# Optimization experiments

Hardware: AMD Instinct MI355X
Metric: run time of the kernel (lower is better)

Reference implementation:

```python
import jax, jax.numpy as jnp
import numpy as np

HIDDEN = 512
HEADS = 8
HEAD_DIM = HIDDEN // HEADS   # 64
MAN_DIM = 256                # manifold_dim = hidden_dim // 2
SCALE = HEAD_DIM ** -0.5


def _c(re, im):
    return jax.lax.complex(re, im)


def setup_inputs() -> dict:
    key = jax.random.key(0)
    ks = jax.random.split(key, 13)
    def w(k, shape, fan_in):
        return (jax.random.normal(k, shape, dtype=jnp.float32) / np.sqrt(fan_in)).astype(jnp.float32)
    B, S = 2, 2048
    return {
        "x": jax.random.normal(ks[0], (B, S, HIDDEN), dtype=jnp.float32),
        "Wq_re": w(ks[1], (HIDDEN, HIDDEN), HIDDEN), "Wq_im": w(ks[2], (HIDDEN, HIDDEN), HIDDEN),
        "Wk_re": w(ks[3], (HIDDEN, HIDDEN), HIDDEN), "Wk_im": w(ks[4], (HIDDEN, HIDDEN), HIDDEN),
        "Wv_re": w(ks[5], (HIDDEN, HIDDEN), HIDDEN), "Wv_im": w(ks[6], (HIDDEN, HIDDEN), HIDDEN),
        "Wm_re": w(ks[7], (HEAD_DIM, MAN_DIM), HEAD_DIM), "Wm_im": w(ks[8], (HEAD_DIM, MAN_DIM), HEAD_DIM),
        "Wmi_re": w(ks[9], (MAN_DIM, HEAD_DIM), MAN_DIM), "Wmi_im": w(ks[10], (MAN_DIM, HEAD_DIM), MAN_DIM),
        "Wo_re": w(ks[11], (HIDDEN, HIDDEN), HIDDEN), "Wo_im": w(ks[12], (HIDDEN, HIDDEN), HIDDEN),
    }


def reference(x, Wq_re, Wq_im, Wk_re, Wk_im, Wv_re, Wv_im,
              Wm_re, Wm_im, Wmi_re, Wmi_im, Wo_re, Wo_im):
    B, S, D = x.shape
    # quantum state preparation: cast to complex, L2-normalize along last dim
    xc = x.astype(jnp.complex64)
    norm = jnp.linalg.norm(xc, axis=-1, keepdims=True)
    xc = xc / norm

    Wq, Wk, Wv = _c(Wq_re, Wq_im), _c(Wk_re, Wk_im), _c(Wv_re, Wv_im)
    Wm, Wmi, Wo = _c(Wm_re, Wm_im), _c(Wmi_re, Wmi_im), _c(Wo_re, Wo_im)

    def heads(t):  # [B,S,D] -> [B,H,S,head_dim]
        return t.reshape(B, S, HEADS, HEAD_DIM).transpose(0, 2, 1, 3)

    q = heads(xc @ Wq)
    k = heads(xc @ Wk)
    v = heads(xc @ Wv)

    # project each head onto the manifold (complex linear)
    qm = jnp.einsum('bhsd,dm->bhsm', q, Wm)
    km = jnp.einsum('bhsd,dm->bhsm', k, Wm)
    vm = jnp.einsum('bhsd,dm->bhsm', v, Wm)

    # Hermitian inner product attention scores; softmax over real part
    scores = jnp.einsum('bhqm,bhkm->bhqk', qm, jnp.conj(km)) * SCALE
    attn = jax.nn.softmax(scores.real, axis=-1).astype(jnp.complex64)

    outm = jnp.einsum('bhqk,bhkm->bhqm', attn, vm)
    out = jnp.einsum('bhsm,md->bhsd', outm, Wmi)        # back to head_dim
    out = out.transpose(0, 2, 1, 3).reshape(B, S, D)    # merge heads
    out = out @ Wo
    # return real/imag stacked as float32 (complex64 output -> [B,S,D,2])
    return jnp.stack([out.real, out.imag], axis=-1)
```

## Files before the change

### kernel.cpp

```cpp
#include <hip/hip_runtime.h>
#include <hip/hip_bf16.h>
#include <stdint.h>


typedef __attribute__((ext_vector_type(8))) short bf16x8;
typedef __attribute__((ext_vector_type(4))) float f32x4;

#define QSCALE 0.18033688011112042f

__device__ __forceinline__ unsigned short f2b(float f) {
    union { float f; unsigned int u; } v; v.f = f;
    unsigned int r = v.u + 0x7fffu + ((v.u >> 16) & 1u);
    return (unsigned short)(r >> 16);
}

__device__ __forceinline__ unsigned int cvtpk(float a, float b) {
    union { __hip_bfloat162 h; unsigned int u; } v;
    v.h = __float22bfloat162_rn(make_float2(a, b));
    return v.u;
}

__device__ __forceinline__ void ld16(void* lds, const void* g) {
    __builtin_amdgcn_global_load_lds(
        (__attribute__((address_space(1))) unsigned int*)(g),
        (__attribute__((address_space(3))) unsigned int*)(lds), 16, 0, 0);
}

__global__ __launch_bounds__(256) void k_prep(
        const float* __restrict__ x, unsigned short* __restrict__ xn,
        const float* __restrict__ s0, const float* __restrict__ s1,
        const float* __restrict__ s2, const float* __restrict__ s3,
        const float* __restrict__ s4, const float* __restrict__ s5,
        const float* __restrict__ s6, const float* __restrict__ s7,
        float* __restrict__ d0, float* __restrict__ d1,
        float* __restrict__ d2, float* __restrict__ d3,
        float* __restrict__ d4, float* __restrict__ d5,
        float* __restrict__ d6, float* __restrict__ d7) {
    __shared__ float tile[64][65];
    if (blockIdx.x < 1024) {
        int row  = blockIdx.x * 4 + (threadIdx.x >> 6);
        int lane = threadIdx.x & 63;
        const float4* xr = (const float4*)(x + (size_t)row * 512);
        float4 a = xr[lane], b = xr[lane + 64];
        float s = a.x*a.x + a.y*a.y + a.z*a.z + a.w*a.w
                + b.x*b.x + b.y*b.y + b.z*b.z + b.w*b.w;
        #pragma unroll
        for (int m = 1; m < 64; m <<= 1) s += __shfl_xor(s, m, 64);
        float inv = 1.0f / sqrtf(s);
        ushort4 o;
        o.x = f2b(a.x*inv); o.y = f2b(a.y*inv); o.z = f2b(a.z*inv); o.w = f2b(a.w*inv);
        *(ushort4*)&xn[(size_t)row*512 + lane*4] = o;
        o.x = f2b(b.x*inv); o.y = f2b(b.y*inv); o.z = f2b(b.z*inv); o.w = f2b(b.w*inv);
        *(ushort4*)&xn[(size_t)row*512 + 256 + lane*4] = o;
        return;
    }
    int bid = blockIdx.x - 1024;
    const float* src; float* dst; int R, C, tr, tc;
    if (bid < 384) {
        int mat = bid >> 6, tl = bid & 63;
        src = (mat==0)?s0:(mat==1)?s1:(mat==2)?s2:(mat==3)?s3:(mat==4)?s4:s5;
        dst = (mat==0)?d0:(mat==1)?d1:(mat==2)?d2:(mat==3)?d3:(mat==4)?d4:d5;
        R = 512; C = 512; tr = tl >> 3; tc = tl & 7;
    } else {
        int mat = (bid - 384) >> 2, tl = (bid - 384) & 3;
        src = mat ? s7 : s6; dst = mat ? d7 : d6;
        R = 64; C = 256; tr = 0; tc = tl;
    }
    int r0 = tr * 64, c0 = tc * 64;
    int tx = threadIdx.x & 63, ty = threadIdx.x >> 6;
    #pragma unroll
    for (int i = 0; i < 16; i++) {
        int r = ty + i*4;
        tile[r][tx] = src[(size_t)(r0 + r)*C + c0 + tx];
    }
    __syncthreads();
    #pragma unroll
    for (int i = 0; i < 16; i++) {
        int r = ty + i*4;
        dst[(size_t)(c0 + r)*R + r0 + tx] = tile[tx][r];
    }
}

__global__ __launch_bounds__(256) void k_gh(const float* __restrict__ Wm_re, const float* __restrict__ Wm_im,
                                            const float* __restrict__ WmT_re, const float* __restrict__ WmT_im,
                                            const float* __restrict__ Wmi_re, const float* __restrict__ Wmi_im,
                                            float* __restrict__ GH) {
    int id = blockIdx.x * 256 + threadIdx.x;
    int mat = id >> 12;
    int a = (id >> 6) & 63, c = id & 63;
    float s = 0.f;
    if (mat < 2) {
        for (int m = 0; m < 256; m++) {
            float ar = Wm_re[a*256+m], ai = Wm_im[a*256+m];
            float br = WmT_re[m*64+c], bi = WmT_im[m*64+c];
            s += (mat == 0) ? (ar*br + ai*bi) : (ai*br - ar*bi);
        }
        GH[id] = s;
    } else {
        for (int m = 0; m < 256; m++) {
            float ar = Wm_re[a*256+m], ai = Wm_im[a*256+m];
            float br = Wmi_re[m*64+c], bi = Wmi_im[m*64+c];
            s += (mat == 2) ? (ar*br - ai*bi) : (ar*bi + ai*br);
        }
        GH[mat*4096 + c*64 + a] = s;
    }
}

__global__ __launch_bounds__(256) void k_pack(
        const float* __restrict__ WqT_re, const float* __restrict__ WqT_im,
        const float* __restrict__ WkT_re, const float* __restrict__ WkT_im,
        const float* __restrict__ WvT_re, const float* __restrict__ WvT_im,
        const float* __restrict__ Wo_re,  const float* __restrict__ Wo_im,
        const float* __restrict__ GH,
        unsigned short* __restrict__ WqkvT, unsigned short* __restrict__ Wbig) {
    if (blockIdx.x < 6144) {
        int id = blockIdx.x * 256 + threadIdx.x;
        int n = id >> 9, k = id & 511;
        float val;
        if (n < 1024) {
            int h = n >> 7, part = (n >> 6) & 1, j = n & 63;
            const float* Gr = GH;
            const float* Gi = GH + 4096;
            const float* qr = WqT_re + (size_t)(h*64)*512 + k;
            const float* qi = WqT_im + (size_t)(h*64)*512 + k;
            float s = 0.f;
            if (part == 0) { for (int d = 0; d < 64; d++) s += qr[d*512]*Gr[d*64+j] - qi[d*512]*Gi[d*64+j]; }
            else           { for (int d = 0; d < 64; d++) s += qr[d*512]*Gi[d*64+j] + qi[d*512]*Gr[d*64+j]; }
            val = s * QSCALE;
        } else if (n < 2048) {
            int m = n - 1024; int h = m >> 7, part = (m >> 6) & 1, j = m & 63;
            val = (part ? WkT_im : WkT_re)[(size_t)(h*64+j)*512 + k];
        } else {
            int m = n - 2048; int h = m >> 7, part = (m >> 6) & 1, j = m & 63;
            val = (part ? WvT_im : WvT_re)[(size_t)(h*64+j)*512 + k];
        }
        WqkvT[id] = f2b(val);
    } else {
        int id = (blockIdx.x - 6144) * 256 + threadIdx.x;
        int np = id >> 10, kk = id & 1023;
        int c = np >> 1, p = np & 1;
        int h = kk >> 7, pp = (kk >> 6) & 1, d = kk & 63;
        const float* HrT = GH + 2*4096;
        const float* HiT = GH + 3*4096;
        float s = 0.f;
        if (p == pp) {
            for (int j = 0; j < 64; j++) {
                float hr = HrT[j*64+d], hi = HiT[j*64+d];
                float wr = Wo_re[(size_t)(h*64+j)*512 + c];
                float wi = Wo_im[(size_t)(h*64+j)*512 + c];
                s += hr*wr - hi*wi;
            }
        } else {
            for (int j = 0; j < 64; j++) {
                float hr = HrT[j*64+d], hi = HiT[j*64+d];
                float wr = Wo_re[(size_t)(h*64+j)*512 + c];
                float wi = Wo_im[(size_t)(h*64+j)*512 + c];
                s += hr*wi + hi*wr;
            }
            if (p == 0) s = -s;
        }
        Wbig[(size_t)np*1024 + kk] = f2b(s);
    }
}

template<int MODE, int MT>
__global__ __launch_bounds__(256, 2) void k_gemm(
        const unsigned short* __restrict__ Ain, const unsigned short* __restrict__ Btin,
        void* __restrict__ Cout, unsigned short* __restrict__ Vt, int K) {
    __shared__ __align__(16) unsigned short Al[MT*32];
    __shared__ __align__(16) unsigned short Bl[128*32];
    const int t = threadIdx.x;
    const int wave = t >> 6, lane = t & 63, quad = lane >> 4, l16 = lane & 15;
    const int wr = wave >> 1, wc = wave & 1;

    const unsigned short* A;
    const unsigned short* Bt;
    unsigned short* Cb = nullptr;
    int m0, n0;
    if (MODE == 0) {
        if (blockIdx.y < 16) {
            A = Ain; Bt = Btin;
            m0 = blockIdx.x * 128; n0 = blockIdx.y * 128;
            Cb = (unsigned short*)Cout;
        } else {
            int idx = (blockIdx.y - 16) * 32 + blockIdx.x;
            int b = idx >> 7, mt = (idx >> 4) & 7, nt = idx & 15;
            A  = Btin + 2048*512;
            Bt = Ain + (size_t)b*2048*512;
            m0 = mt * 128; n0 = nt * 128;
            Cb = Vt + (size_t)b*1024*2048;
        }
    } else {
        A = Ain; Bt = Btin;
        m0 = blockIdx.x * MT; n0 = blockIdx.y * 128;
    }

    f32x4 acc[MT/32][4] = {};
    for (int kt = 0; kt < K; kt += 32) {
        #pragma unroll
        for (int i = 0; i < MT/64; i++) {
            int g = t + i*256, r = g >> 2, gr = g & 3;
            ld16(&Al[g*8], &A[(size_t)(m0 + r)*K + kt + gr*8]);
        }
        #pragma unroll
        for (int i = 0; i < 2; i++) {
            int g = t + i*256, r = g >> 2, gr = g & 3;
            ld16(&Bl[g*8], &Bt[(size_t)(n0 + r)*K + kt + gr*8]);
        }
        __syncthreads();
        bf16x8 af[MT/32], bfr[4];
        #pragma unroll
        for (int rt = 0; rt < MT/32; rt++)
            af[rt] = *(const bf16x8*)&Al[(wr*(MT/2) + rt*16 + l16)*32 + quad*8];
        #pragma unroll
        for (int ct = 0; ct < 4; ct++)
            bfr[ct] = *(const bf16x8*)&Bl[(wc*64 + ct*16 + l16)*32 + quad*8];
        #pragma unroll
        for (int rt = 0; rt < MT/32; rt++)
            #pragma unroll
            for (int ct = 0; ct < 4; ct++)
                acc[rt][ct] = __builtin_amdgcn_mfma_f32_16x16x32_bf16(af[rt], bfr[ct], acc[rt][ct], 0, 0, 0);
        __syncthreads();
    }
    #pragma unroll
    for (int rt = 0; rt < MT/32; rt++) {
        int row = m0 + wr*(MT/2) + rt*16 + quad*4;
        #pragma unroll
        for (int ct = 0; ct < 4; ct++) {
            int col = n0 + wc*64 + ct*16 + l16;
            if (MODE == 0) {
                unsigned int u01 = cvtpk(acc[rt][ct][0], acc[rt][ct][1]);
                unsigned int u23 = cvtpk(acc[rt][ct][2], acc[rt][ct][3]);
                Cb[(size_t)(row+0)*2048 + col] = (unsigned short)(u01);
                Cb[(size_t)(row+1)*2048 + col] = (unsigned short)(u01 >> 16);
                Cb[(size_t)(row+2)*2048 + col] = (unsigned short)(u23);
                Cb[(size_t)(row+3)*2048 + col] = (unsigned short)(u23 >> 16);
            } else {
                float* C = (float*)Cout;
                #pragma unroll
                for (int r = 0; r < 4; r++)
                    C[(size_t)(row + r)*1024 + col] = acc[rt][ct][r];
            }
        }
    }
}

__global__ __launch_bounds__(256, 2) void k_attn(
        const unsigned short* __restrict__ QK,
        const unsigned short* __restrict__ Vt,
        unsigned short* __restrict__ O) {
    __shared__ __align__(16) unsigned short Kl[2][8192];
    __shared__ __align__(16) unsigned short Vl[2][8192];
    __shared__ __align__(16) unsigned short Pl[9216];

    const int t = threadIdx.x, wave = t >> 6, lane = t & 63, quad = lane >> 4, l16 = lane & 15;
    const int bh = blockIdx.x, b = bh >> 3, h = bh & 7;
    const int tok0 = b*2048 + blockIdx.y*128;

    bf16x8 qf[2][4];
    #pragma unroll
    for (int rt = 0; rt < 2; rt++)
        #pragma unroll
        for (int ks = 0; ks < 4; ks++)
            qf[rt][ks] = *(const bf16x8*)&QK[(size_t)(tok0 + wave*32 + rt*16 + l16)*2048 + h*128 + ks*32 + quad*8];

    const int key = t >> 2, gr = t & 3;
    const unsigned short* kp  = QK + (size_t)(b*2048 + key)*2048 + 1024 + h*128 + gr*8;
    const unsigned short* vp0 = Vt + (size_t)(b*1024 + h*128 + key)*2048 + gr*8;
    const unsigned short* vp1 = Vt + (size_t)(b*1024 + h*128 + 64 + key)*2048 + gr*8;

    f32x4 Oacc[2][8] = {};
    float ls[2][4] = {};

    {
        size_t ko = 0;
        #pragma unroll
        for (int i = 0; i < 4; i++) ld16(&Kl[0][(i*256 + t)*8], kp + ko + i*32);
        #pragma unroll
        for (int i = 0; i < 4; i++) ld16(&Vl[0][(i*256 + t)*8], ((i & 1) ? vp1 : vp0) + (i >> 1)*32);
    }
    __syncthreads();

    for (int it = 0; it < 32; it++) {
        const int cur = it & 1;
        if (it < 31) {
            int kt = (it + 1) * 64;
            size_t ko = (size_t)kt * 2048;
            #pragma unroll
            for (int i = 0; i < 4; i++) ld16(&Kl[cur^1][(i*256 + t)*8], kp + ko + i*32);
            #pragma unroll
            for (int i = 0; i < 4; i++) ld16(&Vl[cur^1][(i*256 + t)*8], ((i & 1) ? vp1 : vp0) + kt + (i >> 1)*32);
        }

        f32x4 S[2][4] = {};
        #pragma unroll
        for (int ks = 0; ks < 4; ks++) {
            #pragma unroll
            for (int ct = 0; ct < 4; ct++) {
                bf16x8 kf = *(const bf16x8*)&Kl[cur][ks*2048 + (ct*16 + l16)*32 + quad*8];
                #pragma unroll
                for (int rt = 0; rt < 2; rt++)
                    S[rt][ct] = __builtin_amdgcn_mfma_f32_16x16x32_bf16(qf[rt][ks], kf, S[rt][ct], 0, 0, 0);
            }
        }
        #pragma unroll
        for (int rt = 0; rt < 2; rt++) {
            #pragma unroll
            for (int ct = 0; ct < 4; ct++) {
                float p0 = exp2f(S[rt][ct][0]), p1 = exp2f(S[rt][ct][1]);
                float p2 = exp2f(S[rt][ct][2]), p3 = exp2f(S[rt][ct][3]);
                ls[rt][0] += p0; ls[rt][1] += p1; ls[rt][2] += p2; ls[rt][3] += p3;
                int q = wave*32 + rt*16 + quad*4;
                int base = (ct >> 1)*4608 + (ct & 1)*16 + l16;
                unsigned int u01 = cvtpk(p0, p1);
                unsigned int u23 = cvtpk(p2, p3);
                Pl[base + (q+0)*36] = (unsigned short)(u01);
                Pl[base + (q+1)*36] = (unsigned short)(u01 >> 16);
                Pl[base + (q+2)*36] = (unsigned short)(u23);
                Pl[base + (q+3)*36] = (unsigned short)(u23 >> 16);
            }
        }
        #pragma unroll
        for (int ks2 = 0; ks2 < 2; ks2++) {
            bf16x8 pf[2];
            #pragma unroll
            for (int rt = 0; rt < 2; rt++)
                pf[rt] = *(const bf16x8*)&Pl[ks2*4608 + (wave*32 + rt*16 + l16)*36 + quad*8];
            #pragma unroll
            for (int dt = 0; dt < 8; dt++) {
                bf16x8 vf = *(const bf16x8*)&Vl[cur][ks2*4096 + (dt*16 + l16)*32 + quad*8];
                #pragma unroll
                for (int rt = 0; rt < 2; rt++)
                    Oacc[rt][dt] = __builtin_amdgcn_mfma_f32_16x16x32_bf16(pf[rt], vf, Oacc[rt][dt], 0, 0, 0);
            }
        }
        __syncthreads();
    }

    #pragma unroll
    for (int rt = 0; rt < 2; rt++)
        #pragma unroll
        for (int r = 0; r < 4; r++) {
            float s = ls[rt][r];
            #pragma unroll
            for (int m = 1; m < 16; m <<= 1) s += __shfl_xor(s, m, 64);
            ls[rt][r] = 1.0f / s;
        }
    #pragma unroll
    for (int rt = 0; rt < 2; rt++) {
        int tok = tok0 + wave*32 + rt*16 + quad*4;
        #pragma unroll
        for (int dt = 0; dt < 8; dt++) {
            int col = h*128 + dt*16 + l16;
            unsigned int u01 = cvtpk(Oacc[rt][dt][0]*ls[rt][0], Oacc[rt][dt][1]*ls[rt][1]);
            unsigned int u23 = cvtpk(Oacc[rt][dt][2]*ls[rt][2], Oacc[rt][dt][3]*ls[rt][3]);
            O[(size_t)(tok+0)*1024 + col] = (unsigned short)(u01);
            O[(size_t)(tok+1)*1024 + col] = (unsigned short)(u01 >> 16);
            O[(size_t)(tok+2)*1024 + col] = (unsigned short)(u23);
            O[(size_t)(tok+3)*1024 + col] = (unsigned short)(u23 >> 16);
        }
    }
}

extern "C" void kernel_launch(void* const* d_in, const int* in_sizes, int n_in,
                              void* d_out, int out_size, void* d_ws, size_t ws_size,
                              hipStream_t stream) {
    (void)in_sizes; (void)n_in; (void)out_size; (void)ws_size;
    const float* x      = (const float*)d_in[0];
    const float* Wq_re  = (const float*)d_in[1];
    const float* Wq_im  = (const float*)d_in[2];
    const float* Wk_re  = (const float*)d_in[3];
    const float* Wk_im  = (const float*)d_in[4];
    const float* Wv_re  = (const float*)d_in[5];
    const float* Wv_im  = (const float*)d_in[6];
    const float* Wm_re  = (const float*)d_in[7];
    const float* Wm_im  = (const float*)d_in[8];
    const float* Wmi_re = (const float*)d_in[9];
    const float* Wmi_im = (const float*)d_in[10];
    const float* Wo_re  = (const float*)d_in[11];
    const float* Wo_im  = (const float*)d_in[12];

    char* ws = (char*)d_ws;
    unsigned short* xn    = (unsigned short*)(ws);
    unsigned short* WqkvT = (unsigned short*)(ws + (4u << 20));
    unsigned short* Wbig  = (unsigned short*)(ws + (7u << 20));
    float*          GH    = (float*)         (ws + (9u << 20));
    float*          WmT_re= (float*)         (ws + (9u << 20) + (64u << 10));
    float*          WmT_im= (float*)         (ws + (9u << 20) + (128u << 10));
    unsigned short* QK    = (unsigned short*)(ws + (10u << 20));
    unsigned short* Vt    = (unsigned short*)(ws + (26u << 20));
    unsigned short* Obuf  = (unsigned short*)(ws + (34u << 20));
    float* WqT_re = (float*)(ws + (10u << 20));
    float* WqT_im = (float*)(ws + (11u << 20));
    float* WkT_re = (float*)(ws + (12u << 20));
    float* WkT_im = (float*)(ws + (13u << 20));
    float* WvT_re = (float*)(ws + (14u << 20));
    float* WvT_im = (float*)(ws + (15u << 20));

    k_prep      <<<dim3(1416), dim3(256), 0, stream>>>(
        x, xn,
        Wq_re, Wq_im, Wk_re, Wk_im, Wv_re, Wv_im, Wm_re, Wm_im,
        WqT_re, WqT_im, WkT_re, WkT_im, WvT_re, WvT_im, WmT_re, WmT_im);
    k_gh        <<<dim3(64),   dim3(256), 0, stream>>>(Wm_re, Wm_im, WmT_re, WmT_im, Wmi_re, Wmi_im, GH);
    k_pack      <<<dim3(10240),dim3(256), 0, stream>>>(
        WqT_re, WqT_im, WkT_re, WkT_im, WvT_re, WvT_im, Wo_re, Wo_im, GH, WqkvT, Wbig);
    k_gemm<0,128><<<dim3(32, 24), dim3(256), 0, stream>>>(xn, WqkvT, (void*)QK, Vt, 512);
    k_attn      <<<dim3(16, 16), dim3(256), 0, stream>>>(QK, Vt, Obuf);
    k_gemm<1,64> <<<dim3(64, 8), dim3(256), 0, stream>>>(Obuf, Wbig, d_out, nullptr, 1024);
}
```

Measured before the change: 271.6 us.

## Split attention keys across two wave groups per block and merge partial results

The attention kernel now runs 512 threads per block, split into two groups of four waves that each handle half of the 2048 keys for the same 128 queries. The partial output accumulators and row sums are merged through shared memory at the end. V fragments are now read directly from global memory into registers instead of being staged through LDS. The goal is more waves in flight per block to hide latency on a 256-block grid. The cost is a final merge pass, higher register pressure and uncoalesced V loads from global memory.

```diff
diff --git a/kernel.cpp b/kernel.cpp
--- a/kernel.cpp
+++ b/kernel.cpp
@@ -245,15 +245,17 @@
     }
 }
 
-__global__ __launch_bounds__(256, 2) void k_attn(
+__global__ __launch_bounds__(512, 2) void k_attn(
         const unsigned short* __restrict__ QK,
         const unsigned short* __restrict__ Vt,
         unsigned short* __restrict__ O) {
-    __shared__ __align__(16) unsigned short Kl[2][8192];
-    __shared__ __align__(16) unsigned short Vl[2][8192];
-    __shared__ __align__(16) unsigned short Pl[9216];
-
-    const int t = threadIdx.x, wave = t >> 6, lane = t & 63, quad = lane >> 4, l16 = lane & 15;
+    __shared__ __align__(16) unsigned short Kl[2][2][8192];
+    __shared__ __align__(16) unsigned short Pl[2][9216];
+
+    const int t = threadIdx.x;
+    const int wave = t >> 6, g = wave >> 2, w = wave & 3;
+    const int lane = t & 63, quad = lane >> 4, l16 = lane & 15;
+    const int gt = t & 255;
     const int bh = blockIdx.x, b = bh >> 3, h = bh & 7;
     const int tok0 = b*2048 + blockIdx.y*128;
 
@@ -262,42 +264,41 @@
     for (int rt = 0; rt < 2; rt++)
         #pragma unroll
         for (int ks = 0; ks < 4; ks++)
-            qf[rt][ks] = *(const bf16x8*)&QK[(size_t)(tok0 + wave*32 + rt*16 + l16)*2048 + h*128 + ks*32 + quad*8];
-
-    const int key = t >> 2, gr = t & 3;
-    const unsigned short* kp  = QK + (size_t)(b*2048 + key)*2048 + 1024 + h*128 + gr*8;
-    const unsigned short* vp0 = Vt + (size_t)(b*1024 + h*128 + key)*2048 + gr*8;
-    const unsigned short* vp1 = Vt + (size_t)(b*1024 + h*128 + 64 + key)*2048 + gr*8;
+            qf[rt][ks] = *(const bf16x8*)&QK[(size_t)(tok0 + w*32 + rt*16 + l16)*2048 + h*128 + ks*32 + quad*8];
+
+    const int skey = gt >> 2, sgr = gt & 3;
+    const unsigned short* kp = QK + (size_t)(b*2048 + g*1024 + skey)*2048 + 1024 + h*128 + sgr*8;
+    const unsigned short* vbase = Vt + (size_t)(b*1024 + h*128)*2048 + g*1024;
 
     f32x4 Oacc[2][8] = {};
     float ls[2][4] = {};
 
-    {
-        size_t ko = 0;
-        #pragma unroll
-        for (int i = 0; i < 4; i++) ld16(&Kl[0][(i*256 + t)*8], kp + ko + i*32);
-        #pragma unroll
-        for (int i = 0; i < 4; i++) ld16(&Vl[0][(i*256 + t)*8], ((i & 1) ? vp1 : vp0) + (i >> 1)*32);
-    }
+    #pragma unroll
+    for (int i = 0; i < 4; i++)
+        ld16(&Kl[g][0][(i*256 + gt)*8], kp + i*32);
     __syncthreads();
 
-    for (int it = 0; it < 32; it++) {
+    for (int it = 0; it < 16; it++) {
         const int cur = it & 1;
-        if (it < 31) {
-            int kt = (it + 1) * 64;
-            size_t ko = (size_t)kt * 2048;
-            #pragma unroll
-            for (int i = 0; i < 4; i++) ld16(&Kl[cur^1][(i*256 + t)*8], kp + ko + i*32);
-            #pragma unroll
-            for (int i = 0; i < 4; i++) ld16(&Vl[cur^1][(i*256 + t)*8], ((i & 1) ? vp1 : vp0) + kt + (i >> 1)*32);
-        }
+        const int kt = it * 64;
+        if (it < 15) {
+            #pragma unroll
+            for (int i = 0; i < 4; i++)
+                ld16(&Kl[g][cur^1][(i*256 + gt)*8], kp + (size_t)(kt + 64)*2048 + i*32);
+        }
+        bf16x8 vf[2][8];
+        #pragma unroll
+        for (int ks2 = 0; ks2 < 2; ks2++)
+            #pragma unroll
+            for (int dt = 0; dt < 8; dt++)
+                vf[ks2][dt] = *(const bf16x8*)&vbase[(size_t)(dt*16 + l16)*2048 + kt + ks2*32 + quad*8];
 
         f32x4 S[2][4] = {};
         #pragma unroll
         for (int ks = 0; ks < 4; ks++) {
             #pragma unroll
             for (int ct = 0; ct < 4; ct++) {
-                bf16x8 kf = *(const bf16x8*)&Kl[cur][ks*2048 + (ct*16 + l16)*32 + quad*8];
+                bf16x8 kf = *(const bf16x8*)&Kl[g][cur][ks*2048 + (ct*16 + l16)*32 + quad*8];
                 #pragma unroll
                 for (int rt = 0; rt < 2; rt++)
                     S[rt][ct] = __builtin_amdgcn_mfma_f32_16x16x32_bf16(qf[rt][ks], kf, S[rt][ct], 0, 0, 0);
@@ -310,14 +311,14 @@
                 float p0 = exp2f(S[rt][ct][0]), p1 = exp2f(S[rt][ct][1]);
                 float p2 = exp2f(S[rt][ct][2]), p3 = exp2f(S[rt][ct][3]);
                 ls[rt][0] += p0; ls[rt][1] += p1; ls[rt][2] += p2; ls[rt][3] += p3;
-                int q = wave*32 + rt*16 + quad*4;
+                int q = w*32 + rt*16 + quad*4;
                 int base = (ct >> 1)*4608 + (ct & 1)*16 + l16;
                 unsigned int u01 = cvtpk(p0, p1);
                 unsigned int u23 = cvtpk(p2, p3);
-                Pl[base + (q+0)*36] = (unsigned short)(u01);
-                Pl[base + (q+1)*36] = (unsigned short)(u01 >> 16);
-                Pl[base + (q+2)*36] = (unsigned short)(u23);
-                Pl[base + (q+3)*36] = (unsigned short)(u23 >> 16);
+                Pl[g][base + (q+0)*36] = (unsigned short)(u01);
+                Pl[g][base + (q+1)*36] = (unsigned short)(u01 >> 16);
+                Pl[g][base + (q+2)*36] = (unsigned short)(u23);
+                Pl[g][base + (q+3)*36] = (unsigned short)(u23 >> 16);
             }
         }
         #pragma unroll
@@ -325,14 +326,12 @@
             bf16x8 pf[2];
             #pragma unroll
             for (int rt = 0; rt < 2; rt++)
-                pf[rt] = *(const bf16x8*)&Pl[ks2*4608 + (wave*32 + rt*16 + l16)*36 + quad*8];
-            #pragma unroll
-            for (int dt = 0; dt < 8; dt++) {
-                bf16x8 vf = *(const bf16x8*)&Vl[cur][ks2*4096 + (dt*16 + l16)*32 + quad*8];
+                pf[rt] = *(const bf16x8*)&Pl[g][ks2*4608 + (w*32 + rt*16 + l16)*36 + quad*8];
+            #pragma unroll
+            for (int dt = 0; dt < 8; dt++)
                 #pragma unroll
                 for (int rt = 0; rt < 2; rt++)
-                    Oacc[rt][dt] = __builtin_amdgcn_mfma_f32_16x16x32_bf16(pf[rt], vf, Oacc[rt][dt], 0, 0, 0);
-            }
+                    Oacc[rt][dt] = __builtin_amdgcn_mfma_f32_16x16x32_bf16(pf[rt], vf[ks2][dt], Oacc[rt][dt], 0, 0, 0);
         }
         __syncthreads();
     }
@@ -344,20 +343,47 @@
             float s = ls[rt][r];
             #pragma unroll
             for (int m = 1; m < 16; m <<= 1) s += __shfl_xor(s, m, 64);
-            ls[rt][r] = 1.0f / s;
-        }
-    #pragma unroll
-    for (int rt = 0; rt < 2; rt++) {
-        int tok = tok0 + wave*32 + rt*16 + quad*4;
-        #pragma unroll
-        for (int dt = 0; dt < 8; dt++) {
-            int col = h*128 + dt*16 + l16;
-            unsigned int u01 = cvtpk(Oacc[rt][dt][0]*ls[rt][0], Oacc[rt][dt][1]*ls[rt][1]);
-            unsigned int u23 = cvtpk(Oacc[rt][dt][2]*ls[rt][2], Oacc[rt][dt][3]*ls[rt][3]);
-            O[(size_t)(tok+0)*1024 + col] = (unsigned short)(u01);
-            O[(size_t)(tok+1)*1024 + col] = (unsigned short)(u01 >> 16);
-            O[(size_t)(tok+2)*1024 + col] = (unsigned short)(u23);
-            O[(size_t)(tok+3)*1024 + col] = (unsigned short)(u23 >> 16);
+            ls[rt][r] = s;
+        }
+
+    float* mergeO = (float*)&Kl[0][0][0];
+    float* mergeL = (float*)&Pl[1][0];
+    if (g == 1) {
+        #pragma unroll
+        for (int rt = 0; rt < 2; rt++) {
+            int q = w*32 + rt*16 + quad*4;
+            #pragma unroll
+            for (int r = 0; r < 4; r++) mergeL[q + r] = ls[rt][r];
+            #pragma unroll
+            for (int dt = 0; dt < 8; dt++)
+                #pragma unroll
+                for (int r = 0; r < 4; r++)
+                    mergeO[(q + r)*128 + dt*16 + l16] = Oacc[rt][dt][r];
+        }
+    }
+    __syncthreads();
+    if (g == 0) {
+        #pragma unroll
+        for (int rt = 0; rt < 2; rt++) {
+            int q = w*32 + rt*16 + quad*4;
+            float inv[4];
+            #pragma unroll
+            for (int r = 0; r < 4; r++) inv[r] = 1.0f / (ls[rt][r] + mergeL[q + r]);
+            int tok = tok0 + q;
+            #pragma unroll
+            for (int dt = 0; dt < 8; dt++) {
+                int col = h*128 + dt*16 + l16;
+                float o0 = (Oacc[rt][dt][0] + mergeO[(q+0)*128 + dt*16 + l16]) * inv[0];
+                float o1 = (Oacc[rt][dt][1] + mergeO[(q+1)*128 + dt*16 + l16]) * inv[1];
+                float o2 = (Oacc[rt][dt][2] + mergeO[(q+2)*128 + dt*16 + l16]) * inv[2];
+                float o3 = (Oacc[rt][dt][3] + mergeO[(q+3)*128 + dt*16 + l16]) * inv[3];
+                unsigned int u01 = cvtpk(o0, o1);
+                unsigned int u23 = cvtpk(o2, o3);
+                O[(size_t)(tok+0)*1024 + col] = (unsigned short)(u01);
+                O[(size_t)(tok+1)*1024 + col] = (unsigned short)(u01 >> 16);
+                O[(size_t)(tok+2)*1024 + col] = (unsigned short)(u23);
+                O[(size_t)(tok+3)*1024 + col] = (unsigned short)(u23 >> 16);
+            }
         }
     }
 }
@@ -405,6 +431,6 @@
     k_pack      <<<dim3(10240),dim3(256), 0, stream>>>(
         WqT_re, WqT_im, WkT_re, WkT_im, WvT_re, WvT_im, Wo_re, Wo_im, GH, WqkvT, Wbig);
     k_gemm<0,128><<<dim3(32, 24), dim3(256), 0, stream>>>(xn, WqkvT, (void*)QK, Vt, 512);
-    k_attn      <<<dim3(16, 16), dim3(256), 0, stream>>>(QK, Vt, Obuf);
+    k_attn      <<<dim3(16, 16), dim3(512), 0, stream>>>(QK, Vt, Obuf);
     k_gemm<1,64> <<<dim3(64, 8), dim3(256), 0, stream>>>(Obuf, Wbig, d_out, nullptr, 1024);
 }
```

Result: slower. 284.9 us (+4.9%).

## Split attention keys across two blocks with merge kernel, tile Q-weight packing

Applied to the files above, without the earlier changes.

The attention kernel now splits the key range into two halves, doubling the grid to 512 blocks so more CUs are occupied. Each half writes unnormalised fp32 partial outputs and row sums, and a new merge kernel adds them and normalises. The P staging buffer is halved by interleaving exp/store with the PV MMA per key sub-tile. Separately, the Q-weight packing is tiled through shared memory, and the K/V packing is vectorised, which cuts the pack grid size. The cost is extra fp32 partial traffic (about 32 MB written and read) plus one more launch.

```diff
diff --git a/kernel.cpp b/kernel.cpp
--- a/kernel.cpp
+++ b/kernel.cpp
@@ -113,30 +113,54 @@
         const float* __restrict__ Wo_re,  const float* __restrict__ Wo_im,
         const float* __restrict__ GH,
         unsigned short* __restrict__ WqkvT, unsigned short* __restrict__ Wbig) {
-    if (blockIdx.x < 6144) {
-        int id = blockIdx.x * 256 + threadIdx.x;
-        int n = id >> 9, k = id & 511;
-        float val;
-        if (n < 1024) {
-            int h = n >> 7, part = (n >> 6) & 1, j = n & 63;
-            const float* Gr = GH;
-            const float* Gi = GH + 4096;
-            const float* qr = WqT_re + (size_t)(h*64)*512 + k;
-            const float* qi = WqT_im + (size_t)(h*64)*512 + k;
-            float s = 0.f;
-            if (part == 0) { for (int d = 0; d < 64; d++) s += qr[d*512]*Gr[d*64+j] - qi[d*512]*Gi[d*64+j]; }
-            else           { for (int d = 0; d < 64; d++) s += qr[d*512]*Gi[d*64+j] + qi[d*512]*Gr[d*64+j]; }
-            val = s * QSCALE;
-        } else if (n < 2048) {
-            int m = n - 1024; int h = m >> 7, part = (m >> 6) & 1, j = m & 63;
-            val = (part ? WkT_im : WkT_re)[(size_t)(h*64+j)*512 + k];
-        } else {
-            int m = n - 2048; int h = m >> 7, part = (m >> 6) & 1, j = m & 63;
-            val = (part ? WvT_im : WvT_re)[(size_t)(h*64+j)*512 + k];
-        }
-        WqkvT[id] = f2b(val);
+    const int bid = blockIdx.x, t = threadIdx.x;
+    if (bid < 128) {
+        __shared__ float Wr[64][128];
+        __shared__ float Wi[64][128];
+        const int h = bid >> 4, part = (bid >> 3) & 1, jg = bid & 7;
+        const int w = t >> 6, lane = t & 63;
+        const float* Gr = GH;
+        const float* Gi = GH + 4096;
+        for (int kc = 0; kc < 4; kc++) {
+            #pragma unroll
+            for (int i = 0; i < 8; i++) {
+                int slot = i*256 + t;
+                int d = slot >> 5, kq = slot & 31;
+                *(float4*)&Wr[d][kq*4] = *(const float4*)&WqT_re[(size_t)(h*64+d)*512 + kc*128 + kq*4];
+                *(float4*)&Wi[d][kq*4] = *(const float4*)&WqT_im[(size_t)(h*64+d)*512 + kc*128 + kq*4];
+            }
+            __syncthreads();
+            #pragma unroll
+            for (int rr = 0; rr < 4; rr++) {
+                int task = rr*4 + w;
+                int jloc = task >> 1, kh = task & 1;
+                int j = jg*8 + jloc;
+                float acc = 0.f;
+                #pragma unroll
+                for (int d = 0; d < 64; d++) {
+                    float gr = Gr[d*64 + j], gi = Gi[d*64 + j];
+                    float wr = Wr[d][kh*64 + lane], wi = Wi[d][kh*64 + lane];
+                    acc += part ? (wr*gi + wi*gr) : (wr*gr - wi*gi);
+                }
+                int n = h*128 + part*64 + j;
+                int k = kc*128 + kh*64 + lane;
+                WqkvT[(size_t)n*512 + k] = f2b(acc * QSCALE);
+            }
+            __syncthreads();
+        }
+    } else if (bid < 1152) {
+        int bp = bid - 128;
+        int row = bp*2 + (t >> 7);
+        int k = (t & 127) * 4;
+        int m = (row < 1024) ? row : (row - 1024);
+        int hh = m >> 7, part = (m >> 6) & 1, j = m & 63;
+        const float* src = (row < 1024) ? (part ? WkT_im : WkT_re)
+                                        : (part ? WvT_im : WvT_re);
+        float4 v = *(const float4*)&src[(size_t)(hh*64 + j)*512 + k];
+        ushort4 o; o.x = f2b(v.x); o.y = f2b(v.y); o.z = f2b(v.z); o.w = f2b(v.w);
+        *(ushort4*)&WqkvT[(size_t)(1024 + row)*512 + k] = o;
     } else {
-        int id = (blockIdx.x - 6144) * 256 + threadIdx.x;
+        int id = (bid - 1152) * 256 + t;
         int np = id >> 10, kk = id & 1023;
         int c = np >> 1, p = np & 1;
         int h = kk >> 7, pp = (kk >> 6) & 1, d = kk & 63;
@@ -248,48 +272,44 @@
 __global__ __launch_bounds__(256, 2) void k_attn(
         const unsigned short* __restrict__ QK,
         const unsigned short* __restrict__ Vt,
-        unsigned short* __restrict__ O) {
+        float* __restrict__ Opart,
+        float* __restrict__ Lpart) {
     __shared__ __align__(16) unsigned short Kl[2][8192];
     __shared__ __align__(16) unsigned short Vl[2][8192];
-    __shared__ __align__(16) unsigned short Pl[9216];
-
-    const int t = threadIdx.x, wave = t >> 6, lane = t & 63, quad = lane >> 4, l16 = lane & 15;
+    __shared__ __align__(16) unsigned short Pl[4608];
+
+    const int t = threadIdx.x, w = t >> 6, lane = t & 63, quad = lane >> 4, l16 = lane & 15;
     const int bh = blockIdx.x, b = bh >> 3, h = bh & 7;
-    const int tok0 = b*2048 + blockIdx.y*128;
+    const int qb = blockIdx.y & 15, half = blockIdx.y >> 4;
+    const int tok0 = b*2048 + qb*128;
 
     bf16x8 qf[2][4];
     #pragma unroll
     for (int rt = 0; rt < 2; rt++)
         #pragma unroll
         for (int ks = 0; ks < 4; ks++)
-            qf[rt][ks] = *(const bf16x8*)&QK[(size_t)(tok0 + wave*32 + rt*16 + l16)*2048 + h*128 + ks*32 + quad*8];
-
-    const int key = t >> 2, gr = t & 3;
-    const unsigned short* kp  = QK + (size_t)(b*2048 + key)*2048 + 1024 + h*128 + gr*8;
-    const unsigned short* vp0 = Vt + (size_t)(b*1024 + h*128 + key)*2048 + gr*8;
-    const unsigned short* vp1 = Vt + (size_t)(b*1024 + h*128 + 64 + key)*2048 + gr*8;
+            qf[rt][ks] = *(const bf16x8*)&QK[(size_t)(tok0 + w*32 + rt*16 + l16)*2048 + h*128 + ks*32 + quad*8];
+
+    const unsigned short* kp = QK + (size_t)(b*2048 + half*1024 + (t >> 2))*2048 + 1024 + h*128 + (t & 3)*8;
+    const unsigned short* vp = Vt + (size_t)(b*1024 + h*128 + (t >> 2))*2048 + half*1024 + (t & 3)*8;
 
     f32x4 Oacc[2][8] = {};
     float ls[2][4] = {};
 
-    {
-        size_t ko = 0;
-        #pragma unroll
-        for (int i = 0; i < 4; i++) ld16(&Kl[0][(i*256 + t)*8], kp + ko + i*32);
-        #pragma unroll
-        for (int i = 0; i < 4; i++) ld16(&Vl[0][(i*256 + t)*8], ((i & 1) ? vp1 : vp0) + (i >> 1)*32);
-    }
+    #pragma unroll
+    for (int i = 0; i < 4; i++) ld16(&Kl[0][(i*256 + t)*8], kp + i*32);
+    #pragma unroll
+    for (int i = 0; i < 4; i++) ld16(&Vl[0][(i*256 + t)*8], vp + (i & 1)*131072 + (i >> 1)*32);
     __syncthreads();
 
-    for (int it = 0; it < 32; it++) {
+    for (int it = 0; it < 16; it++) {
         const int cur = it & 1;
-        if (it < 31) {
-            int kt = (it + 1) * 64;
-            size_t ko = (size_t)kt * 2048;
-            #pragma unroll
-            for (int i = 0; i < 4; i++) ld16(&Kl[cur^1][(i*256 + t)*8], kp + ko + i*32);
-            #pragma unroll
-            for (int i = 0; i < 4; i++) ld16(&Vl[cur^1][(i*256 + t)*8], ((i & 1) ? vp1 : vp0) + kt + (i >> 1)*32);
+        if (it < 15) {
+            int kt2 = (it + 1) * 64;
+            #pragma unroll
+            for (int i = 0; i < 4; i++) ld16(&Kl[cur^1][(i*256 + t)*8], kp + (size_t)kt2*2048 + i*32);
+            #pragma unroll
+            for (int i = 0; i < 4; i++) ld16(&Vl[cur^1][(i*256 + t)*8], vp + kt2 + (i & 1)*131072 + (i >> 1)*32);
         }
 
         f32x4 S[2][4] = {};
@@ -304,28 +324,29 @@
             }
         }
         #pragma unroll
-        for (int rt = 0; rt < 2; rt++) {
-            #pragma unroll
-            for (int ct = 0; ct < 4; ct++) {
-                float p0 = exp2f(S[rt][ct][0]), p1 = exp2f(S[rt][ct][1]);
-                float p2 = exp2f(S[rt][ct][2]), p3 = exp2f(S[rt][ct][3]);
-                ls[rt][0] += p0; ls[rt][1] += p1; ls[rt][2] += p2; ls[rt][3] += p3;
-                int q = wave*32 + rt*16 + quad*4;
-                int base = (ct >> 1)*4608 + (ct & 1)*16 + l16;
-                unsigned int u01 = cvtpk(p0, p1);
-                unsigned int u23 = cvtpk(p2, p3);
-                Pl[base + (q+0)*36] = (unsigned short)(u01);
-                Pl[base + (q+1)*36] = (unsigned short)(u01 >> 16);
-                Pl[base + (q+2)*36] = (unsigned short)(u23);
-                Pl[base + (q+3)*36] = (unsigned short)(u23 >> 16);
-            }
-        }
-        #pragma unroll
         for (int ks2 = 0; ks2 < 2; ks2++) {
+            #pragma unroll
+            for (int rt = 0; rt < 2; rt++) {
+                #pragma unroll
+                for (int ct2 = 0; ct2 < 2; ct2++) {
+                    int ct = ks2*2 + ct2;
+                    float p0 = exp2f(S[rt][ct][0]), p1 = exp2f(S[rt][ct][1]);
+                    float p2 = exp2f(S[rt][ct][2]), p3 = exp2f(S[rt][ct][3]);
+                    ls[rt][0] += p0; ls[rt][1] += p1; ls[rt][2] += p2; ls[rt][3] += p3;
+                    int q = w*32 + rt*16 + quad*4;
+                    int base = ct2*16 + l16;
+                    unsigned int u01 = cvtpk(p0, p1);
+                    unsigned int u23 = cvtpk(p2, p3);
+                    Pl[base + (q+0)*36] = (unsigned short)(u01);
+                    Pl[base + (q+1)*36] = (unsigned short)(u01 >> 16);
+                    Pl[base + (q+2)*36] = (unsigned short)(u23);
+                    Pl[base + (q+3)*36] = (unsigned short)(u23 >> 16);
+                }
+            }
             bf16x8 pf[2];
             #pragma unroll
             for (int rt = 0; rt < 2; rt++)
-                pf[rt] = *(const bf16x8*)&Pl[ks2*4608 + (wave*32 + rt*16 + l16)*36 + quad*8];
+                pf[rt] = *(const bf16x8*)&Pl[(w*32 + rt*16 + l16)*36 + quad*8];
             #pragma unroll
             for (int dt = 0; dt < 8; dt++) {
                 bf16x8 vf = *(const bf16x8*)&Vl[cur][ks2*4096 + (dt*16 + l16)*32 + quad*8];
@@ -344,21 +365,47 @@
             float s = ls[rt][r];
             #pragma unroll
             for (int m = 1; m < 16; m <<= 1) s += __shfl_xor(s, m, 64);
-            ls[rt][r] = 1.0f / s;
-        }
+            ls[rt][r] = s;
+        }
+    float* Op = Opart + (size_t)half*4096*1024;
+    float* Lp = Lpart + (size_t)half*32768;
     #pragma unroll
     for (int rt = 0; rt < 2; rt++) {
-        int tok = tok0 + wave*32 + rt*16 + quad*4;
+        int q = w*32 + rt*16 + quad*4;
+        int tok = tok0 + q;
+        if (l16 == 0) {
+            #pragma unroll
+            for (int r = 0; r < 4; r++) Lp[(size_t)(tok + r)*8 + h] = ls[rt][r];
+        }
         #pragma unroll
         for (int dt = 0; dt < 8; dt++) {
             int col = h*128 + dt*16 + l16;
-            unsigned int u01 = cvtpk(Oacc[rt][dt][0]*ls[rt][0], Oacc[rt][dt][1]*ls[rt][1]);
-            unsigned int u23 = cvtpk(Oacc[rt][dt][2]*ls[rt][2], Oacc[rt][dt][3]*ls[rt][3]);
-            O[(size_t)(tok+0)*1024 + col] = (unsigned short)(u01);
-            O[(size_t)(tok+1)*1024 + col] = (unsigned short)(u01 >> 16);
-            O[(size_t)(tok+2)*1024 + col] = (unsigned short)(u23);
-            O[(size_t)(tok+3)*1024 + col] = (unsigned short)(u23 >> 16);
-        }
+            #pragma unroll
+            for (int r = 0; r < 4; r++)
+                Op[(size_t)(tok + r)*1024 + col] = Oacc[rt][dt][r];
+        }
+    }
+}
+
+__global__ __launch_bounds__(256) void k_merge(const float* __restrict__ Opart,
+                                               const float* __restrict__ Lpart,
+                                               unsigned short* __restrict__ O) {
+    int tid = blockIdx.x * 256 + threadIdx.x;
+    #pragma unroll
+    for (int rep = 0; rep < 2; rep++) {
+        int slot = tid + rep * 524288;
+        int tok = slot >> 8, cg = slot & 255, h = cg >> 5;
+        float l0 = Lpart[(size_t)tok*8 + h];
+        float l1 = Lpart[32768 + (size_t)tok*8 + h];
+        float inv = 1.0f / (l0 + l1);
+        float4 a = ((const float4*)Opart)[slot];
+        float4 b = ((const float4*)Opart)[1048576 + slot];
+        unsigned int u01 = cvtpk((a.x + b.x)*inv, (a.y + b.y)*inv);
+        unsigned int u23 = cvtpk((a.z + b.z)*inv, (a.w + b.w)*inv);
+        ushort4 o;
+        o.x = (unsigned short)u01; o.y = (unsigned short)(u01 >> 16);
+        o.z = (unsigned short)u23; o.w = (unsigned short)(u23 >> 16);
+        ((ushort4*)O)[slot] = o;
     }
 }
 
@@ -390,6 +437,8 @@
     unsigned short* QK    = (unsigned short*)(ws + (10u << 20));
     unsigned short* Vt    = (unsigned short*)(ws + (26u << 20));
     unsigned short* Obuf  = (unsigned short*)(ws + (34u << 20));
+    float*          Opart = (float*)         (ws + (42u << 20));
+    float*          Lpart = (float*)         (ws + (74u << 20));
     float* WqT_re = (float*)(ws + (10u << 20));
     float* WqT_im = (float*)(ws + (11u << 20));
     float* WkT_re = (float*)(ws + (12u << 20));
@@ -402,9 +451,10 @@
         Wq_re, Wq_im, Wk_re, Wk_im, Wv_re, Wv_im, Wm_re, Wm_im,
         WqT_re, WqT_im, WkT_re, WkT_im, WvT_re, WvT_im, WmT_re, WmT_im);
     k_gh        <<<dim3(64),   dim3(256), 0, stream>>>(Wm_re, Wm_im, WmT_re, WmT_im, Wmi_re, Wmi_im, GH);
-    k_pack      <<<dim3(10240),dim3(256), 0, stream>>>(
+    k_pack      <<<dim3(5248), dim3(256), 0, stream>>>(
         WqT_re, WqT_im, WkT_re, WkT_im, WvT_re, WvT_im, Wo_re, Wo_im, GH, WqkvT, Wbig);
     k_gemm<0,128><<<dim3(32, 24), dim3(256), 0, stream>>>(xn, WqkvT, (void*)QK, Vt, 512);
-    k_attn      <<<dim3(16, 16), dim3(256), 0, stream>>>(QK, Vt, Obuf);
+    k_attn      <<<dim3(16, 32), dim3(256), 0, stream>>>(QK, Vt, Opart, Lpart);
+    k_merge     <<<dim3(2048), dim3(256), 0, stream>>>(Opart, Lpart, Obuf);
     k_gemm<1,64> <<<dim3(64, 8), dim3(256), 0, stream>>>(Obuf, Wbig, d_out, nullptr, 1024);
 }
```

New measurement: 465.5 us. +71.4%, slower.
